# Optimization experiments

Measured on AMD Instinct MI355X. Metric: run time of the kernel, lower is better.

Reference implementation:

```python
import jax, jax.numpy as jnp
import numpy as np

N, K, C_S, C_Z, C_G, H, NUM_RBF = 768, 32, 384, 128, 16, 4, 64
E = N * K
DH = C_Z // H  # 32
LN_EPS = 1e-5
DIST_EPS = 1e-8


def _rbf(D, D_min=0.0, D_max=20.0, D_count=NUM_RBF):
    # Gaussian radial basis expansion (GVP/ProteinMPNN style)
    mu = jnp.linspace(D_min, D_max, D_count, dtype=D.dtype)
    sigma = (D_max - D_min) / D_count
    return jnp.exp(-(((D[..., None] - mu) / sigma) ** 2))


def setup_inputs() -> dict:
    key = jax.random.key(0)
    ks = jax.random.split(key, 24)
    node_features = jax.random.normal(ks[0], (N, C_S), dtype=jnp.float32)
    node_trans = jax.random.uniform(ks[1], (N, 3), dtype=jnp.float32) * 30.0  # coords in a 30A box
    edge_features = jax.random.normal(ks[2], (E, C_Z), dtype=jnp.float32)
    src = jax.random.randint(ks[3], (E,), 0, N)
    dst = jnp.repeat(jnp.arange(N), K)  # sorted-by-destination layout (assume_sorted)
    edge_index = jnp.stack([src, dst]).astype(jnp.int64)

    def lin(k, fan_in, fan_out, scale=0.02):
        return jax.random.normal(k, (fan_in, fan_out), dtype=jnp.float32) * scale

    return {
        "node_features": node_features,
        "node_trans": node_trans,
        "edge_features": edge_features,
        "edge_index": edge_index,
        "w_left": lin(ks[4], C_S, C_G), "b_left": jnp.zeros((C_G,), jnp.float32),
        "w_right": lin(ks[5], C_S, C_G), "b_right": jnp.zeros((C_G,), jnp.float32),
        "w_bgate": lin(ks[6], C_G * C_G, C_Z), "b_bgate": jnp.zeros((C_Z,), jnp.float32),
        "w_dist": lin(ks[7], NUM_RBF, C_Z), "b_dist": jnp.zeros((C_Z,), jnp.float32),
        "w_tobias": lin(ks[8], C_Z, H),
        "ln_g": jnp.ones((C_Z,), jnp.float32), "ln_b": jnp.zeros((C_Z,), jnp.float32),
        "w_q": lin(ks[9], C_Z, C_Z), "b_q": jnp.zeros((C_Z,), jnp.float32),
        "w_kv": lin(ks[10], C_Z, 2 * C_Z), "b_kv": jnp.zeros((2 * C_Z,), jnp.float32),
        "w_out": lin(ks[11], C_Z, C_Z), "b_out": jnp.zeros((C_Z,), jnp.float32),
        "w_ogate": lin(ks[12], C_Z, C_Z), "b_ogate": jnp.zeros((C_Z,), jnp.float32),
    }


def reference(node_features, node_trans, edge_features, edge_index,
              w_left, b_left, w_right, b_right, w_bgate, b_bgate,
              w_dist, b_dist, w_tobias, ln_g, ln_b,
              w_q, b_q, w_kv, b_kv, w_out, b_out, w_ogate, b_ogate):
    # sparse -> knn graph (edges pre-sorted by destination, exactly K per node)
    knn_idx = edge_index[0].reshape(N, K)            # [N, K] source node of each neighbor edge
    feat = edge_features.reshape(N, K, C_Z)          # [N, K, c_z]

    # LayerNorm over c_z
    mu = feat.mean(-1, keepdims=True)
    var = feat.var(-1, keepdims=True)
    z = (feat - mu) * jax.lax.rsqrt(var + LN_EPS) * ln_g + ln_b  # [N, K, c_z]

    # outer-product gating bias
    nl = node_features @ w_left + b_left             # [N, c_gate_s]
    nr = node_features @ w_right + b_right
    e1 = nl[knn_idx]                                 # [N, K, c_gate_s]
    e2 = nr[knn_idx]
    edge3 = jnp.einsum('nik,njl->nijkl', e1, e2).reshape(N, K, K, C_G * C_G)
    gate = edge3 @ w_bgate + b_bgate                 # [N, K, K, c_z]

    # RBF distance bias
    t = node_trans[knn_idx]                          # [N, K, 3]
    diff = t[:, :, None, :] - t[:, None, :, :] + DIST_EPS
    dist = jnp.sqrt(jnp.sum(diff * diff, axis=-1))   # [N, K, K]
    db = _rbf(dist) @ w_dist + b_dist                # [N, K, K, c_z]
    bias = (jax.nn.sigmoid(gate) * db) @ w_tobias    # [N, K, K, H]

    # attention over the K neighbors of each node
    q = (z @ w_q + b_q).reshape(N, K, H, DH)
    kv = z @ w_kv + b_kv
    k_ = kv[..., :C_Z].reshape(N, K, H, DH)
    v = kv[..., C_Z:].reshape(N, K, H, DH)
    scores = jnp.einsum('nihd,njhd->nhij', q, k_) / jnp.sqrt(jnp.asarray(DH, q.dtype))
    scores = scores + bias.transpose(0, 3, 1, 2)     # [N, H, K, K] (mask all-True -> no -inf term)
    p = jax.nn.softmax(scores, axis=-1)
    o = jnp.einsum('nhij,njhd->nihd', p, v).reshape(N, K, C_Z)

    # output gate + projection, then knn -> sparse (identity reshape: full mask, sorted edges)
    o = o * jax.nn.sigmoid(z @ w_ogate + b_ogate)
    out = (o @ w_out + b_out).reshape(E, C_Z)
    return out
```

## Files before the change

kernel.cpp:

```cpp
#include <hip/hip_runtime.h>

#define NN   768
#define KKN  32
#define CS   384
#define CZ   128
#define CG   16
#define NH   4
#define DHD  32
#define NRBF 64
#define EE   (NN*KKN)

#define RBF_STEP    (20.0f/63.0f)
#define RBF_INVSTEP (63.0f/20.0f)
#define RBF_INVSIG  3.2f
#define RBF_SI      (RBF_STEP*RBF_INVSIG)

typedef __attribute__((ext_vector_type(8))) short bf16x8;
typedef __attribute__((ext_vector_type(4))) float f32x4;

__device__ __forceinline__ float bfl(unsigned int u){ return __uint_as_float(u << 16); }
__device__ __forceinline__ float bfh(unsigned int u){ return __uint_as_float(u & 0xFFFF0000u); }
__device__ __forceinline__ unsigned int packbf(float a, float b){
  unsigned int r;
  asm("v_cvt_pk_bf16_f32 %0, %1, %2" : "=v"(r) : "v"(a), "v"(b));
  return r;
}
__device__ __forceinline__ float fastrcp(float x){
  float r;
  asm("v_rcp_f32 %0, %1" : "=v"(r) : "v"(x));
  return r;
}
__device__ __forceinline__ float sigm(float x){ return fastrcp(1.0f + __expf(-x)); }

__global__ __launch_bounds__(256) void k1_pre(
    const float* __restrict__ nf, const float* __restrict__ ef,
    const float* __restrict__ wl, const float* __restrict__ bl,
    const float* __restrict__ wr, const float* __restrict__ br,
    const float* __restrict__ lng, const float* __restrict__ lnb,
    float* __restrict__ nlw, float* __restrict__ nrw,
    unsigned short* __restrict__ zw,
    const float* __restrict__ wq, const float* __restrict__ wkv,
    const float* __restrict__ wog, const float* __restrict__ wout,
    const float* __restrict__ wd, const float* __restrict__ wt,
    const float* __restrict__ wb, const float* __restrict__ bgf,
    unsigned short* __restrict__ wqkvogT, unsigned short* __restrict__ woutT,
    unsigned short* __restrict__ wdT, unsigned short* __restrict__ wtT,
    unsigned short* __restrict__ wbP, unsigned short* __restrict__ bgP)
{
  int b = blockIdx.x, t = threadIdx.x;
  if (b < 1536){
    int rl = t >> 4, l16 = t & 15;
    size_t e = (size_t)b*16 + rl;
    const float4* row = (const float4*)(ef + e*CZ);
    float4 x0 = row[l16*2], x1 = row[l16*2+1];
    float v[8] = {x0.x,x0.y,x0.z,x0.w,x1.x,x1.y,x1.z,x1.w};
    float s = 0.f, q = 0.f;
    #pragma unroll
    for (int u=0;u<8;u++){ s += v[u]; q += v[u]*v[u]; }
    #pragma unroll
    for (int m=1;m<16;m<<=1){ s += __shfl_xor(s,m); q += __shfl_xor(q,m); }
    float mean = s*(1.f/128.f);
    float var  = q*(1.f/128.f) - mean*mean;
    float rs = rsqrtf(var + 1e-5f);
    int c0 = l16*8;
    unsigned int pk[4];
    #pragma unroll
    for (int u=0;u<4;u++){
      float z0 = (v[2*u]  -mean)*rs*lng[c0+2*u]   + lnb[c0+2*u];
      float z1 = (v[2*u+1]-mean)*rs*lng[c0+2*u+1] + lnb[c0+2*u+1];
      pk[u] = packbf(z0,z1);
    }
    ((uint4*)(zw + e*CZ))[l16] = make_uint4(pk[0],pk[1],pk[2],pk[3]);
  } else if (b < 2304){
    int blk2 = b - 1536;
    int seg = blk2 / 96;
    int within = blk2 - seg*96;
    int gid = within*256 + t;
    int side = (gid >= 12288) ? 1 : 0;
    int idx = gid - side*12288;
    int nd = idx >> 4, c = idx & 15;
    const float* w = side ? wr : wl;
    float acc = (seg==0) ? (side ? br[c] : bl[c]) : 0.f;
    const float* nrow = nf + (size_t)nd*CS;
    int kb = seg*48;
    #pragma unroll 4
    for (int k=kb;k<kb+48;k++) acc += nrow[k]*w[k*CG+c];
    atomicAdd((side? nrw : nlw)+idx, acc);
  } else {
    int id = (b - 2304)*256 + t;
    float v[8];
    if (id < 8192){
      int c = id & 511, g = id >> 9;
      const float* src; int ld, col;
      if (c < 128){ src = wq; ld = 128; col = c; }
      else if (c < 384){ src = wkv; ld = 256; col = c-128; }
      else { src = wog; ld = 128; col = c-384; }
      #pragma unroll
      for (int j=0;j<8;j++) v[j] = src[(size_t)(g*8+j)*ld + col];
      *(uint4*)(wqkvogT + c*128 + ((g + c)&15)*8) = make_uint4(
        packbf(v[0],v[1]),packbf(v[2],v[3]),packbf(v[4],v[5]),packbf(v[6],v[7]));
    } else if (id < 10240){
      int l = id - 8192; int c = l & 127, g = l >> 7;
      #pragma unroll
      for (int j=0;j<8;j++) v[j] = wout[(size_t)(g*8+j)*128 + c];
      *(uint4*)(woutT + c*128 + ((g + c)&15)*8) = make_uint4(
        packbf(v[0],v[1]),packbf(v[2],v[3]),packbf(v[4],v[5]),packbf(v[6],v[7]));
    } else if (id < 11392){
      int l = id - 10240; int c = l & 127, g = l >> 7;
      #pragma unroll
      for (int j=0;j<8;j++) v[j] = (g<8) ? wd[(size_t)(g*8+j)*128 + c] : 0.f;
      *(uint4*)(wdT + c*72 + g*8) = make_uint4(
        packbf(v[0],v[1]),packbf(v[2],v[3]),packbf(v[4],v[5]),packbf(v[6],v[7]));
    } else if (id < 11460){
      int l = id - 11392; int h = l / 17, g = l % 17;
      #pragma unroll
      for (int j=0;j<8;j++){ int cc = g*8+j; v[j] = (cc<128)? wt[cc*4 + h] : 0.f; }
      *(uint4*)(wtT + h*136 + g*8) = make_uint4(
        packbf(v[0],v[1]),packbf(v[2],v[3]),packbf(v[4],v[5]),packbf(v[6],v[7]));
    } else if (id < 15556){
      int l2 = id - 11460;
      int c = l2 >> 5, sl = l2 & 31;
      int kl0 = sl*8;
      #pragma unroll
      for (int j=0;j<8;j++) v[j] = wb[(size_t)(kl0+j)*128 + c];
      *(uint4*)(wbP + c*256 + kl0) = make_uint4(
        packbf(v[0],v[1]),packbf(v[2],v[3]),packbf(v[4],v[5]),packbf(v[6],v[7]));
    } else if (id < 15684){
      int c = id - 15556;
      *(uint4*)(bgP + c*8) = make_uint4(packbf(bgf[c], 0.f), 0u, 0u, 0u);
    }
  }
}

__global__ __launch_bounds__(256) void k1b_sprep(
    const float* __restrict__ nlw, const float* __restrict__ nrw,
    const unsigned short* __restrict__ wbP,
    unsigned short* __restrict__ S_all, unsigned short* __restrict__ nrb)
{
  int n = blockIdx.x, t = threadIdx.x;
  float e1[16];
  #pragma unroll
  for (int k=0;k<16;k++) e1[k] = nlw[n*CG + k];
  int c = t>>1, l0 = (t&1)*8;
  float S[8];
  #pragma unroll
  for (int u=0;u<8;u++) S[u]=0.f;
  const unsigned short* wrow = wbP + c*256 + l0;
  #pragma unroll 4
  for (int k=0;k<16;k++){
    uint4 wv = *(const uint4*)(wrow + k*16);
    float wf[8] = { bfl(wv.x), bfh(wv.x), bfl(wv.y), bfh(wv.y),
                    bfl(wv.z), bfh(wv.z), bfl(wv.w), bfh(wv.w) };
    float ev = e1[k];
    #pragma unroll
    for (int u=0;u<8;u++) S[u] = fmaf(ev, wf[u], S[u]);
  }
  *(uint4*)(S_all + (size_t)n*2048 + c*16 + l0) = make_uint4(
    packbf(S[0],S[1]), packbf(S[2],S[3]), packbf(S[4],S[5]), packbf(S[6],S[7]));
  if (t < 8){
    *(unsigned int*)(nrb + n*CG + 2*t) = packbf(nrw[n*CG + 2*t], nrw[n*CG + 2*t + 1]);
  }
}

__global__ __launch_bounds__(256,4) void k23_fused(
    const long long* __restrict__ eidx, const float* __restrict__ trans,
    const unsigned short* __restrict__ S_all, const unsigned short* __restrict__ nrb,
    const unsigned short* __restrict__ wdTg, const unsigned short* __restrict__ wtTg,
    const unsigned short* __restrict__ bgP, const float* __restrict__ bd,
    const unsigned short* __restrict__ zw,
    const unsigned short* __restrict__ wqkvogT, const unsigned short* __restrict__ woutT,
    const float* __restrict__ bq, const float* __restrict__ bkv, const float* __restrict__ bog,
    const float* __restrict__ bout, float* __restrict__ out)
{
  int n = blockIdx.x, t = threadIdx.x;
  int wave = t>>6, lane = t&63, q = lane>>4, l15 = lane&15;
  int w = wave;

  __shared__ __align__(16) char smem[40960];
  float* biasF          = (float*)smem;
  unsigned short* Xb    = (unsigned short*)(smem + 16384);
  unsigned short* rbfb  = (unsigned short*)(smem + 25088);
  float* dsm            = (float*)(smem + 29696);
  float* t3s            = (float*)(smem + 33792);
  int*   srcs           = (int*)(smem + 34304);

  f32x4 zero4 = {0.f,0.f,0.f,0.f};
  uint4 uz = make_uint4(0,0,0,0);

  if (t < 32) srcs[t] = (int)eidx[(size_t)n*KKN + t];
  __syncthreads();
  if (t < 32){ int s = srcs[t];
    t3s[t*4]=trans[s*3]; t3s[t*4+1]=trans[s*3+1]; t3s[t*4+2]=trans[s*3+2]; }
  uint4 wdf[2][2];
  #pragma unroll
  for (int mt=0;mt<2;mt++){
    #pragma unroll
    for (int ks=0;ks<2;ks++)
      wdf[mt][ks] = *(const uint4*)(wdTg + (wave*32+mt*16+l15)*72 + ks*32 + q*8);
  }
  uint4 wtf[4];
  #pragma unroll
  for (int ks=0;ks<4;ks++)
    wtf[ks] = *(const uint4*)(wtTg + (l15&3)*136 + ks*32 + q*8);
  uint4 aBias[2];
  #pragma unroll
  for (int mt=0;mt<2;mt++)
    aBias[mt] = (q == 2) ? *(const uint4*)(bgP + (wave*32+mt*16+l15)*8) : uz;
  uint4 bE[2];
  #pragma unroll
  for (int nt=0;nt<2;nt++){
    int jn = srcs[nt*16 + l15];
    bE[nt] = (q < 2) ? *(const uint4*)(nrb + jn*CG + q*8)
                     : (q == 2 ? make_uint4(0x3F80u,0u,0u,0u) : uz);
  }
  uint4 aS[2], aSn[2];
  {
    int s0 = srcs[0];
    #pragma unroll
    for (int mt=0;mt<2;mt++)
      aS[mt] = (q < 2) ? *(const uint4*)(S_all + (size_t)s0*2048 + (wave*32+mt*16+l15)*16 + q*8)
                       : aBias[mt];
  }
  __syncthreads();
  #pragma unroll
  for (int u=0;u<4;u++){
    int idx = t + u*256;
    int di = idx >> 5, j = idx & 31;
    float dx=t3s[di*4]  -t3s[j*4]  +1e-8f;
    float dy=t3s[di*4+1]-t3s[j*4+1]+1e-8f;
    float dz=t3s[di*4+2]-t3s[j*4+2]+1e-8f;
    dsm[di*32+j]=sqrtf(dx*dx+dy*dy+dz*dz);
  }
  __syncthreads();

  int jr = t>>3, sl = t&7;
  int c0base = wave*32 + q*4;
  float4 bdv[2];
  #pragma unroll
  for (int mt=0;mt<2;mt++) bdv[mt] = *(const float4*)(bd + c0base + mt*16);

  #pragma unroll 1
  for (int ii=0; ii<32; ii++){
    {
      float dI = dsm[ii*32 + jr]*RBF_INVSIG;
      float e[8];
      #pragma unroll
      for (int u=0;u<8;u++){
        float x = fmaf((float)(sl*8+u), -RBF_SI, dI);
        e[u] = __expf(-x*x);
      }
      *(uint4*)&rbfb[jr*72 + sl*8] = make_uint4(
        packbf(e[0],e[1]), packbf(e[2],e[3]), packbf(e[4],e[5]), packbf(e[6],e[7]));
    }
    if (ii < 31){
      int s_n = srcs[ii+1];
      #pragma unroll
      for (int mt=0;mt<2;mt++)
        aSn[mt] = (q < 2) ? *(const uint4*)(S_all + (size_t)s_n*2048 + (wave*32+mt*16+l15)*16 + q*8)
                          : aBias[mt];
    }
    __syncthreads();

    f32x4 ga[2][2], da[2][2];
    #pragma unroll
    for(int a=0;a<2;a++){
      #pragma unroll
      for(int b2=0;b2<2;b2++){ ga[a][b2]=zero4; da[a][b2]=zero4; }
    }
    #pragma unroll
    for(int mt=0;mt<2;mt++){
      #pragma unroll
      for(int nt=0;nt<2;nt++)
        ga[mt][nt] = __builtin_amdgcn_mfma_f32_16x16x32_bf16(
          *(const bf16x8*)&aS[mt], *(const bf16x8*)&bE[nt], ga[mt][nt], 0,0,0);
    }
    #pragma unroll
    for(int ks=0;ks<2;ks++){
      bf16x8 bR[2];
      #pragma unroll
      for(int nt=0;nt<2;nt++) bR[nt] = *(const bf16x8*)&rbfb[(nt*16+l15)*72 + ks*32 + q*8];
      #pragma unroll
      for(int mt=0;mt<2;mt++){
        #pragma unroll
        for(int nt=0;nt<2;nt++)
          da[mt][nt] = __builtin_amdgcn_mfma_f32_16x16x32_bf16(
            *(const bf16x8*)&wdf[mt][ks], bR[nt], da[mt][nt], 0,0,0);
      }
    }
    #pragma unroll
    for(int mt=0;mt<2;mt++){
      int c0 = c0base + mt*16;
      float4 bv = bdv[mt];
      #pragma unroll
      for(int nt=0;nt<2;nt++){
        float x0 = fastrcp(1.f + __expf(-ga[mt][nt][0]))*(da[mt][nt][0]+bv.x);
        float x1 = fastrcp(1.f + __expf(-ga[mt][nt][1]))*(da[mt][nt][1]+bv.y);
        float x2 = fastrcp(1.f + __expf(-ga[mt][nt][2]))*(da[mt][nt][2]+bv.z);
        float x3 = fastrcp(1.f + __expf(-ga[mt][nt][3]))*(da[mt][nt][3]+bv.w);
        *(uint2*)&Xb[(nt*16+l15)*136 + c0] = make_uint2(packbf(x0,x1), packbf(x2,x3));
      }
    }
    __syncthreads();

    if (wave < 2){
      f32x4 bacc = {0.f,0.f,0.f,0.f};
      #pragma unroll
      for(int ks=0;ks<4;ks++){
        bf16x8 bX = *(const bf16x8*)&Xb[(wave*16+l15)*136 + ks*32 + q*8];
        bacc = __builtin_amdgcn_mfma_f32_16x16x32_bf16(*(const bf16x8*)&wtf[ks], bX, bacc, 0,0,0);
      }
      if (q==0){
        int j = wave*16 + l15;
        float* base = biasF + ii*32 + j;
        base[0] = bacc[0]; base[1024] = bacc[1]; base[2048] = bacc[2]; base[3072] = bacc[3];
      }
    }
    aS[0] = aSn[0]; aS[1] = aSn[1];
  }
  __syncthreads();

  float bbv[2][4][2];
  {
    const float* bbl = biasF + w*1024;
    #pragma unroll
    for (int mt=0;mt<2;mt++){
      #pragma unroll
      for (int rg=0;rg<4;rg++){
        int i = mt*16 + q*4 + rg;
        bbv[mt][rg][0] = bbl[i*32 + l15];
        bbv[mt][rg][1] = bbl[i*32 + 16 + l15];
      }
    }
  }
  bf16x8 zfr[2][4];
  #pragma unroll
  for (int nt=0;nt<2;nt++){
    const unsigned short* zr = zw + ((size_t)n*32 + nt*16 + l15)*128;
    #pragma unroll
    for (int ks=0;ks<4;ks++) zfr[nt][ks] = *(const bf16x8*)(zr + ks*32 + q*8);
  }
  const float* bseg = (w==0)? bq : (w==1)? bkv : (w==2)? (bkv+128) : bog;
  __syncthreads();

  for (int r=0;r<8;r++){
    float4 bv = *(const float4*)(bseg + r*16 + q*4);
    f32x4 acc0 = zero4, acc1 = zero4;
    int cg = w*128 + r*16 + l15;
    const unsigned short* wrow = wqkvogT + cg*128;
    #pragma unroll
    for (int ks=0;ks<4;ks++){
      bf16x8 af = *(const bf16x8*)(wrow + (((ks*4+q) + cg)&15)*8);
      acc0 = __builtin_amdgcn_mfma_f32_16x16x32_bf16(af, zfr[0][ks], acc0, 0,0,0);
      acc1 = __builtin_amdgcn_mfma_f32_16x16x32_bf16(af, zfr[1][ks], acc1, 0,0,0);
    }
    #pragma unroll
    for (int nt=0;nt<2;nt++){
      f32x4 a = nt? acc1 : acc0;
      float v0,v1,v2,v3;
      if (w==3){ v0=sigm(a[0]+bv.x); v1=sigm(a[1]+bv.y); v2=sigm(a[2]+bv.z); v3=sigm(a[3]+bv.w); }
      else     { v0=a[0]+bv.x; v1=a[1]+bv.y; v2=a[2]+bv.z; v3=a[3]+bv.w; }
      int i = nt*16 + l15;
      if (w==2){
        unsigned short* vt = (unsigned short*)(smem + 16384) + (r*16 + q*4)*32 + i;
        unsigned int u01 = packbf(v0,v1), u23 = packbf(v2,v3);
        vt[0]  = (unsigned short)u01;  vt[32] = (unsigned short)(u01>>16);
        vt[64] = (unsigned short)u23;  vt[96] = (unsigned short)(u23>>16);
      } else {
        int blk = ((r*2 + (q>>1)) + i) & 15;
        *(uint2*)(smem + w*8192 + i*256 + blk*16 + (q&1)*8) = make_uint2(packbf(v0,v1), packbf(v2,v3));
      }
    }
  }
  __syncthreads();

  f32x4 sc4[2][2];
  {
    uint4 aQ[2], bK[2];
    #pragma unroll
    for (int mt=0;mt<2;mt++){
      int row = mt*16 + l15;
      aQ[mt] = *(const uint4*)(smem + row*256 + (((w*4+q) + row)&15)*16);
    }
    #pragma unroll
    for (int nt=0;nt<2;nt++){
      int row = nt*16 + l15;
      bK[nt] = *(const uint4*)(smem + 8192 + row*256 + (((w*4+q) + row)&15)*16);
    }
    #pragma unroll
    for (int mt=0;mt<2;mt++){
      #pragma unroll
      for (int nt=0;nt<2;nt++)
        sc4[mt][nt] = __builtin_amdgcn_mfma_f32_16x16x32_bf16(
          *(const bf16x8*)&aQ[mt], *(const bf16x8*)&bK[nt], zero4, 0,0,0);
    }
  }
  float inv_[2][4];
  #pragma unroll
  for (int mt=0;mt<2;mt++){
    #pragma unroll
    for (int rg=0;rg<4;rg++){
      sc4[mt][0][rg] = fmaf(sc4[mt][0][rg], 0.17677669529663687f, bbv[mt][rg][0]);
      sc4[mt][1][rg] = fmaf(sc4[mt][1][rg], 0.17677669529663687f, bbv[mt][rg][1]);
      float m = fmaxf(sc4[mt][0][rg], sc4[mt][1][rg]);
      m = fmaxf(m, __shfl_xor(m,1));
      m = fmaxf(m, __shfl_xor(m,2));
      m = fmaxf(m, __shfl_xor(m,4));
      m = fmaxf(m, __shfl_xor(m,8));
      sc4[mt][0][rg] = __expf(sc4[mt][0][rg] - m);
      sc4[mt][1][rg] = __expf(sc4[mt][1][rg] - m);
      float s = sc4[mt][0][rg] + sc4[mt][1][rg];
      s += __shfl_xor(s,1); s += __shfl_xor(s,2);
      s += __shfl_xor(s,4); s += __shfl_xor(s,8);
      inv_[mt][rg] = fastrcp(s);
    }
  }
  unsigned short* Pl = (unsigned short*)(smem + 32768 + w*2048);
  #pragma unroll
  for (int mt=0;mt<2;mt++){
    #pragma unroll
    for (int nt=0;nt<2;nt++){
      unsigned int u01 = packbf(sc4[mt][nt][0], sc4[mt][nt][1]);
      unsigned int u23 = packbf(sc4[mt][nt][2], sc4[mt][nt][3]);
      unsigned short* pp = Pl + (mt*16 + q*4)*32 + nt*16 + l15;
      pp[0]  = (unsigned short)u01;  pp[32] = (unsigned short)(u01>>16);
      pp[64] = (unsigned short)u23;  pp[96] = (unsigned short)(u23>>16);
    }
  }
  __syncthreads();

  f32x4 ov[2][2];
  {
    uint4 aP[2], bV[2];
    #pragma unroll
    for (int mt=0;mt<2;mt++)
      aP[mt] = *(const uint4*)(Pl + (mt*16 + l15)*32 + q*8);
    #pragma unroll
    for (int nt2=0;nt2<2;nt2++)
      bV[nt2] = *(const uint4*)((unsigned short*)(smem + 16384) + (w*32 + nt2*16 + l15)*32 + q*8);
    #pragma unroll
    for (int mt=0;mt<2;mt++){
      #pragma unroll
      for (int nt2=0;nt2<2;nt2++)
        ov[mt][nt2] = __builtin_amdgcn_mfma_f32_16x16x32_bf16(
          *(const bf16x8*)&aP[mt], *(const bf16x8*)&bV[nt2], zero4, 0,0,0);
    }
  }
  #pragma unroll
  for (int mt=0;mt<2;mt++){
    #pragma unroll
    for (int nt2=0;nt2<2;nt2++){
      #pragma unroll
      for (int rg=0;rg<4;rg++){
        int i = mt*16 + q*4 + rg;
        int c = w*32 + nt2*16 + l15;
        int off = i*256 + (((c>>3) + i)&15)*16 + (c&7)*2;
        unsigned short gus = *(const unsigned short*)(smem + 24576 + off);
        float g = __uint_as_float(((unsigned int)gus) << 16);
        float yv = ov[mt][nt2][rg] * inv_[mt][rg] * g;
        *(unsigned short*)(smem + off) = (unsigned short)packbf(yv, yv);
      }
    }
  }
  __syncthreads();

  bf16x8 yfr[2][4];
  #pragma unroll
  for (int mt=0;mt<2;mt++){
    int row = mt*16 + l15;
    #pragma unroll
    for (int ks=0;ks<4;ks++)
      yfr[mt][ks] = *(const bf16x8*)(smem + row*256 + (((ks*4+q) + row)&15)*16);
  }
  #pragma unroll
  for (int r2=0;r2<2;r2++){
    int c0 = (r2*4 + w)*16;
    int cg2 = c0 + l15;
    const unsigned short* orow = woutT + cg2*128;
    f32x4 oa0 = zero4, oa1 = zero4;
    #pragma unroll
    for (int ks=0;ks<4;ks++){
      bf16x8 bf = *(const bf16x8*)(orow + (((ks*4+q) + cg2)&15)*8);
      oa0 = __builtin_amdgcn_mfma_f32_16x16x32_bf16(yfr[0][ks], bf, oa0, 0,0,0);
      oa1 = __builtin_amdgcn_mfma_f32_16x16x32_bf16(yfr[1][ks], bf, oa1, 0,0,0);
    }
    float bov = bout[cg2];
    #pragma unroll
    for (int mt=0;mt<2;mt++){
      f32x4 oa = mt? oa1 : oa0;
      #pragma unroll
      for (int rg=0; rg<4; rg++){
        int i = mt*16 + q*4 + rg;
        out[((size_t)n*32 + i)*128 + cg2] = oa[rg] + bov;
      }
    }
  }
}

extern "C" void kernel_launch(void* const* d_in, const int* in_sizes, int n_in,
                              void* d_out, int out_size, void* d_ws, size_t ws_size,
                              hipStream_t stream)
{
  const float* nf  = (const float*)d_in[0];
  const float* tr  = (const float*)d_in[1];
  const float* ef  = (const float*)d_in[2];
  const long long* ei = (const long long*)d_in[3];
  const float* wl  = (const float*)d_in[4];  const float* bl  = (const float*)d_in[5];
  const float* wr  = (const float*)d_in[6];  const float* br  = (const float*)d_in[7];
  const float* wbg = (const float*)d_in[8];  const float* bbg = (const float*)d_in[9];
  const float* wdi = (const float*)d_in[10]; const float* bdi = (const float*)d_in[11];
  const float* wtb = (const float*)d_in[12];
  const float* lng = (const float*)d_in[13]; const float* lnb = (const float*)d_in[14];
  const float* wq  = (const float*)d_in[15]; const float* bq  = (const float*)d_in[16];
  const float* wkv = (const float*)d_in[17]; const float* bkv = (const float*)d_in[18];
  const float* wo  = (const float*)d_in[19]; const float* bo  = (const float*)d_in[20];
  const float* wog = (const float*)d_in[21]; const float* bog = (const float*)d_in[22];
  float* outp = (float*)d_out;
  float* ws = (float*)d_ws;
  float* nlw = ws;
  float* nrw = ws + 12288;
  unsigned short* zw      = (unsigned short*)(ws + 3170304);
  unsigned short* wqkvogT = (unsigned short*)(ws + 4743168);
  unsigned short* woutT   = (unsigned short*)(ws + 4775936);
  unsigned short* wdTg    = (unsigned short*)(ws + 4784128);
  unsigned short* wtTg    = (unsigned short*)(ws + 4788736);
  unsigned short* bgPg    = wtTg + 544;
  unsigned short* wbPg    = (unsigned short*)(ws + 4789824);
  unsigned short* S_all   = (unsigned short*)(ws + 4806208);
  unsigned short* nrb     = (unsigned short*)(ws + 5592640);

  hipMemsetAsync(nlw, 0, 24576*sizeof(float), stream);
  hipLaunchKernelGGL(k1_pre, dim3(2366), dim3(256), 0, stream,
                     nf, ef, wl, bl, wr, br, lng, lnb, nlw, nrw, zw,
                     wq, wkv, wog, wo, wdi, wtb, wbg, bbg,
                     wqkvogT, woutT, wdTg, wtTg, wbPg, bgPg);
  hipLaunchKernelGGL(k1b_sprep, dim3(768), dim3(256), 0, stream,
                     nlw, nrw, wbPg, S_all, nrb);
  hipLaunchKernelGGL(k23_fused, dim3(768), dim3(256), 0, stream,
                     ei, tr, S_all, nrb, wdTg, wtTg, bgPg, bdi,
                     zw, wqkvogT, woutT, bq, bkv, bog, bo, outp);
}
```

Before: 188.0 us.

## Fuse node projection and S-prep into pre-kernel, drop memset and atomics

The separate k1b_sprep kernel and the memset are removed. Each of the 768 node blocks in k1_pre now computes its left and right projections with shuffle reductions, keeps them in shared memory, and immediately forms the S_all bilinear product directly from fp32 w_bgate. This removes one kernel launch, the memset, the atomics and the bf16 wbP repack step. The trade-off is that every block rereads the strided fp32 w_bgate instead of a packed bf16 copy.

```diff
diff --git a/kernel.cpp b/kernel.cpp
--- a/kernel.cpp
+++ b/kernel.cpp
@@ -37,7 +37,7 @@
     const float* __restrict__ wl, const float* __restrict__ bl,
     const float* __restrict__ wr, const float* __restrict__ br,
     const float* __restrict__ lng, const float* __restrict__ lnb,
-    float* __restrict__ nlw, float* __restrict__ nrw,
+    unsigned short* __restrict__ S_all, unsigned short* __restrict__ nrb,
     unsigned short* __restrict__ zw,
     const float* __restrict__ wq, const float* __restrict__ wkv,
     const float* __restrict__ wog, const float* __restrict__ wout,
@@ -45,9 +45,10 @@
     const float* __restrict__ wb, const float* __restrict__ bgf,
     unsigned short* __restrict__ wqkvogT, unsigned short* __restrict__ woutT,
     unsigned short* __restrict__ wdT, unsigned short* __restrict__ wtT,
-    unsigned short* __restrict__ wbP, unsigned short* __restrict__ bgP)
+    unsigned short* __restrict__ bgP)
 {
   int b = blockIdx.x, t = threadIdx.x;
+  __shared__ float nlS[16], nrS[16];
   if (b < 1536){
     int rl = t >> 4, l16 = t & 15;
     size_t e = (size_t)b*16 + rl;
@@ -72,20 +73,43 @@
     }
     ((uint4*)(zw + e*CZ))[l16] = make_uint4(pk[0],pk[1],pk[2],pk[3]);
   } else if (b < 2304){
-    int blk2 = b - 1536;
-    int seg = blk2 / 96;
-    int within = blk2 - seg*96;
-    int gid = within*256 + t;
-    int side = (gid >= 12288) ? 1 : 0;
-    int idx = gid - side*12288;
-    int nd = idx >> 4, c = idx & 15;
-    const float* w = side ? wr : wl;
-    float acc = (seg==0) ? (side ? br[c] : bl[c]) : 0.f;
-    const float* nrow = nf + (size_t)nd*CS;
-    int kb = seg*48;
-    #pragma unroll 4
-    for (int k=kb;k<kb+48;k++) acc += nrow[k]*w[k*CG+c];
-    atomicAdd((side? nrw : nlw)+idx, acc);
+    int n2 = b - 1536;
+    {
+      int c = t >> 4, sl = t & 15;
+      const float* nrow = nf + (size_t)n2*CS + sl*24;
+      float aL = 0.f, aR = 0.f;
+      #pragma unroll 4
+      for (int u=0; u<24; u++){
+        float x = nrow[u];
+        int k = sl*24 + u;
+        aL = fmaf(x, wl[k*CG + c], aL);
+        aR = fmaf(x, wr[k*CG + c], aR);
+      }
+      #pragma unroll
+      for (int m=1;m<16;m<<=1){ aL += __shfl_xor(aL,m); aR += __shfl_xor(aR,m); }
+      if (sl == 0){ nlS[c] = aL + bl[c]; nrS[c] = aR + br[c]; }
+    }
+    __syncthreads();
+    float e1[16];
+    #pragma unroll
+    for (int k=0;k<16;k++) e1[k] = nlS[k];
+    int c2 = t>>1, l0 = (t&1)*8;
+    float S[8];
+    #pragma unroll
+    for (int u=0;u<8;u++) S[u]=0.f;
+    #pragma unroll 2
+    for (int k=0;k<16;k++){
+      float ev = e1[k];
+      const float* wrow = wb + (size_t)(k*16 + l0)*128 + c2;
+      #pragma unroll
+      for (int u=0;u<8;u++)
+        S[u] = fmaf(ev, wrow[u*128], S[u]);
+    }
+    *(uint4*)(S_all + (size_t)n2*2048 + c2*16 + l0) = make_uint4(
+      packbf(S[0],S[1]), packbf(S[2],S[3]), packbf(S[4],S[5]), packbf(S[6],S[7]));
+    if (t < 8){
+      *(unsigned int*)(nrb + n2*CG + 2*t) = packbf(nrS[2*t], nrS[2*t+1]);
+    }
   } else {
     int id = (b - 2304)*256 + t;
     float v[8];
@@ -117,48 +141,10 @@
       for (int j=0;j<8;j++){ int cc = g*8+j; v[j] = (cc<128)? wt[cc*4 + h] : 0.f; }
       *(uint4*)(wtT + h*136 + g*8) = make_uint4(
         packbf(v[0],v[1]),packbf(v[2],v[3]),packbf(v[4],v[5]),packbf(v[6],v[7]));
-    } else if (id < 15556){
-      int l2 = id - 11460;
-      int c = l2 >> 5, sl = l2 & 31;
-      int kl0 = sl*8;
-      #pragma unroll
-      for (int j=0;j<8;j++) v[j] = wb[(size_t)(kl0+j)*128 + c];
-      *(uint4*)(wbP + c*256 + kl0) = make_uint4(
-        packbf(v[0],v[1]),packbf(v[2],v[3]),packbf(v[4],v[5]),packbf(v[6],v[7]));
-    } else if (id < 15684){
-      int c = id - 15556;
+    } else if (id < 11588){
+      int c = id - 11460;
       *(uint4*)(bgP + c*8) = make_uint4(packbf(bgf[c], 0.f), 0u, 0u, 0u);
     }
-  }
-}
-
-__global__ __launch_bounds__(256) void k1b_sprep(
-    const float* __restrict__ nlw, const float* __restrict__ nrw,
-    const unsigned short* __restrict__ wbP,
-    unsigned short* __restrict__ S_all, unsigned short* __restrict__ nrb)
-{
-  int n = blockIdx.x, t = threadIdx.x;
-  float e1[16];
-  #pragma unroll
-  for (int k=0;k<16;k++) e1[k] = nlw[n*CG + k];
-  int c = t>>1, l0 = (t&1)*8;
-  float S[8];
-  #pragma unroll
-  for (int u=0;u<8;u++) S[u]=0.f;
-  const unsigned short* wrow = wbP + c*256 + l0;
-  #pragma unroll 4
-  for (int k=0;k<16;k++){
-    uint4 wv = *(const uint4*)(wrow + k*16);
-    float wf[8] = { bfl(wv.x), bfh(wv.x), bfl(wv.y), bfh(wv.y),
-                    bfl(wv.z), bfh(wv.z), bfl(wv.w), bfh(wv.w) };
-    float ev = e1[k];
-    #pragma unroll
-    for (int u=0;u<8;u++) S[u] = fmaf(ev, wf[u], S[u]);
-  }
-  *(uint4*)(S_all + (size_t)n*2048 + c*16 + l0) = make_uint4(
-    packbf(S[0],S[1]), packbf(S[2],S[3]), packbf(S[4],S[5]), packbf(S[6],S[7]));
-  if (t < 8){
-    *(unsigned int*)(nrb + n*CG + 2*t) = packbf(nrw[n*CG + 2*t], nrw[n*CG + 2*t + 1]);
   }
 }
 
@@ -516,25 +502,19 @@
   const float* wog = (const float*)d_in[21]; const float* bog = (const float*)d_in[22];
   float* outp = (float*)d_out;
   float* ws = (float*)d_ws;
-  float* nlw = ws;
-  float* nrw = ws + 12288;
   unsigned short* zw      = (unsigned short*)(ws + 3170304);
   unsigned short* wqkvogT = (unsigned short*)(ws + 4743168);
   unsigned short* woutT   = (unsigned short*)(ws + 4775936);
   unsigned short* wdTg    = (unsigned short*)(ws + 4784128);
   unsigned short* wtTg    = (unsigned short*)(ws + 4788736);
   unsigned short* bgPg    = wtTg + 544;
-  unsigned short* wbPg    = (unsigned short*)(ws + 4789824);
   unsigned short* S_all   = (unsigned short*)(ws + 4806208);
   unsigned short* nrb     = (unsigned short*)(ws + 5592640);
 
-  hipMemsetAsync(nlw, 0, 24576*sizeof(float), stream);
   hipLaunchKernelGGL(k1_pre, dim3(2366), dim3(256), 0, stream,
-                     nf, ef, wl, bl, wr, br, lng, lnb, nlw, nrw, zw,
+                     nf, ef, wl, bl, wr, br, lng, lnb, S_all, nrb, zw,
                      wq, wkv, wog, wo, wdi, wtb, wbg, bbg,
-                     wqkvogT, woutT, wdTg, wtTg, wbPg, bgPg);
-  hipLaunchKernelGGL(k1b_sprep, dim3(768), dim3(256), 0, stream,
-                     nlw, nrw, wbPg, S_all, nrb);
+                     wqkvogT, woutT, wdTg, wtTg, bgPg);
   hipLaunchKernelGGL(k23_fused, dim3(768), dim3(256), 0, stream,
                      ei, tr, S_all, nrb, wdTg, wtTg, bgPg, bdi,
                      zw, wqkvogT, woutT, bq, bkv, bog, bo, outp);
```

Result: slower. 217.5 us (+15.7%).
